# Kernel tuning notes

Hardware: AMD Instinct MI355X
Metric: run time of the kernel (lower is better)

Reference implementation:

```python
import jax, jax.numpy as jnp
import numpy as np
import math

E = 8192        # number of hyperedges in the batch
IN_DIM = 256
OUT_DIM = 128


def setup_inputs() -> dict:
    key = jax.random.key(0)
    k1, k2, k3, k4 = jax.random.split(key, 4)
    node_embeddings = jax.random.normal(k1, (E, IN_DIM), dtype=jnp.float32)
    # xavier_uniform-like scale for the projection weights
    lim = 1.414 * math.sqrt(6.0 / (IN_DIM + OUT_DIM))
    query_weight = jax.random.uniform(k2, (IN_DIM, OUT_DIM), minval=-lim, maxval=lim, dtype=jnp.float32)
    key_weight = jax.random.uniform(k3, (IN_DIM, OUT_DIM), minval=-lim, maxval=lim, dtype=jnp.float32)
    # binary hypergraph connectivity mask [E, E]; diagonal forced to 1 so no row is fully masked
    mask = jax.random.randint(k4, (E, E), 0, 2, dtype=jnp.int32)
    mask = mask.at[jnp.arange(E), jnp.arange(E)].set(1)
    return {
        "node_embeddings": node_embeddings,
        "query_weight": query_weight,
        "key_weight": key_weight,
        "attention_mask": mask,
    }


def reference(node_embeddings, query_weight, key_weight, attention_mask):
    # QK projections: [E, in] x [in, out] -> [E, out]
    q = node_embeddings @ query_weight
    k = node_embeddings @ key_weight
    # scaled scores [E, E]
    scores = (q @ k.T) / jnp.sqrt(jnp.asarray(OUT_DIM, dtype=q.dtype))
    # masked_fill(mask == 0, -inf)
    scores = jnp.where(attention_mask == 0, jnp.asarray(-jnp.inf, dtype=scores.dtype), scores)
    probs = jax.nn.softmax(scores, axis=1)
    # output aggregates the KEY projections (as in the original code)
    return probs @ k
```

## Files before the change

### kernel.cpp

```cpp
#include <hip/hip_runtime.h>
#include <stdint.h>

#define E_N 8192
#define SPLIT 8
#define CH 16
#define QBLK 64

typedef unsigned short u16;
typedef unsigned int u32;
typedef unsigned long long u64;
typedef __attribute__((ext_vector_type(4))) float f32x4;
typedef __attribute__((ext_vector_type(8))) short bf16x8;
typedef __attribute__((ext_vector_type(4))) unsigned int u32x4;
typedef __attribute__((ext_vector_type(2))) unsigned int u32x2;

union V16 { u32x4 q; bf16x8 h; u16 u[8]; };

static __device__ __forceinline__ u16 f2bf(float f) {
  union { float f; unsigned u; } c; c.f = f;
  unsigned r = c.u + 0x7FFFu + ((c.u >> 16) & 1u);
  return (u16)(r >> 16);
}

constexpr float QS = 1.4426950408889634f / 11.313708498984761f;

__global__ void k_wt(const float* __restrict__ Wq, const float* __restrict__ Wk,
                     u16* __restrict__ wt) {
  int idx = blockIdx.x * 256 + threadIdx.x;
  int mat = idx >> 15, rem = idx & 32767;
  float v = mat ? Wk[rem] : Wq[rem];
  int d = rem >> 7, c = rem & 127;
  wt[(mat * 128 + c) * 256 + d] = f2bf(v);
}

__launch_bounds__(256)
__global__ void k_proj(const float* __restrict__ X, const u16* __restrict__ wt,
                       u16* __restrict__ qg, u16* __restrict__ kg) {
  __shared__ __align__(16) char Xs[64 * 512];
  const int tid = threadIdx.x;
  const int wid = tid >> 6, lane = tid & 63, g = lane >> 4, l15 = lane & 15;
  const int r0 = blockIdx.x * 64;
#pragma unroll
  for (int i = 0; i < 16; ++i) {
    int s = tid + 256 * i;
    int row = s >> 6, c4 = (s & 63) << 2;
    f32x4 v = *(const f32x4*)(X + (size_t)(r0 + row) * 256 + c4);
    u32x2 pk;
    pk[0] = f2bf(v[0]) | ((unsigned)f2bf(v[1]) << 16);
    pk[1] = f2bf(v[2]) | ((unsigned)f2bf(v[3]) << 16);
    *(u32x2*)(Xs + (((row << 9) + (c4 << 1)) ^ ((row & 7) << 4))) = pk;
  }
  __syncthreads();
  bf16x8 xa[8];
  const int arow = wid * 16 + l15;
#pragma unroll
  for (int ks = 0; ks < 8; ++ks) {
    V16 t; t.q = *(const u32x4*)(Xs + (((arow << 9) + (ks << 6) + (g << 4)) ^ ((l15 & 7) << 4)));
    xa[ks] = t.h;
  }
  const f32x4 zero4 = {0.f, 0.f, 0.f, 0.f};
  f32x4 acc[16];
#pragma unroll
  for (int i = 0; i < 16; ++i) acc[i] = zero4;
#pragma unroll
  for (int ct = 0; ct < 16; ++ct) {
    int mat = ct >> 3, c = ((ct & 7) << 4) + l15;
#pragma unroll
    for (int ks = 0; ks < 8; ++ks) {
      V16 b; b.q = *(const u32x4*)(wt + ((mat * 128 + c) * 256 + (ks << 5) + (g << 3)));
      acc[ct] = __builtin_amdgcn_mfma_f32_16x16x32_bf16(xa[ks], b.h, acc[ct], 0, 0, 0);
    }
  }
#pragma unroll
  for (int ct = 0; ct < 16; ++ct) {
    int mat = ct >> 3, c = ((ct & 7) << 4) + l15;
#pragma unroll
    for (int r = 0; r < 4; ++r) {
      int row = r0 + wid * 16 + 4 * g + r;
      float v = acc[ct][r];
      if (mat == 0) qg[row * 128 + c] = f2bf(v * QS);
      else          kg[row * 128 + c] = f2bf(v);
    }
  }
}

__global__ void k_kt(const u16* __restrict__ kg, u16* __restrict__ ktg) {
  __shared__ __align__(16) u16 Ts[64 * 66];
  const int tid = threadIdx.x;
  const int b = blockIdx.x;
  const int r0 = (b >> 1) * 64, c0 = (b & 1) * 64;
#pragma unroll
  for (int i = 0; i < 2; ++i) {
    int s = tid + 256 * i;
    int row = s >> 3, seg = s & 7;
    u32x4 v = *(const u32x4*)(kg + (size_t)(r0 + row) * 128 + c0 + seg * 8);
    unsigned* dst = (unsigned*)((char*)Ts + row * 132 + seg * 16);
    dst[0] = v[0]; dst[1] = v[1]; dst[2] = v[2]; dst[3] = v[3];
  }
  __syncthreads();
#pragma unroll
  for (int i = 0; i < 2; ++i) {
    int s = tid + 256 * i;
    int oc = s >> 3, seg2 = s & 7;
    u16 t[8];
#pragma unroll
    for (int j = 0; j < 8; ++j) t[j] = Ts[(seg2 * 8 + j) * 66 + oc];
    u32x4 o;
    o[0] = t[0] | ((unsigned)t[1] << 16);
    o[1] = t[2] | ((unsigned)t[3] << 16);
    o[2] = t[4] | ((unsigned)t[5] << 16);
    o[3] = t[6] | ((unsigned)t[7] << 16);
    *(u32x4*)(ktg + (size_t)(c0 + oc) * E_N + r0 + seg2 * 8) = o;
  }
}

#define BARRIER() { asm volatile("s_waitcnt lgkmcnt(0)" ::: "memory"); \
                    __builtin_amdgcn_s_barrier(); }

#define LOADREGS(KV1)                                                           \
  {                                                                             \
    const u16* kp = kgp + (size_t)(KV1) * 128;                                  \
    kr0 = *(const u32x4*)(kp);                                                  \
    kr1 = *(const u32x4*)(kp + 16 * 128);                                       \
    kr2 = *(const u32x4*)(kp + 32 * 128);                                       \
    kr3 = *(const u32x4*)(kp + 48 * 128);                                       \
    const u16* tp = ktp + (KV1);                                                \
    tr0 = *(const u32x4*)(tp);                                                  \
    tr1 = *(const u32x4*)(tp + 32 * E_N);                                       \
    tr2 = *(const u32x4*)(tp + 64 * E_N);                                       \
    tr3 = *(const u32x4*)(tp + 96 * E_N);                                       \
  }

#define WRITELDS(KW, TW)                                                        \
  {                                                                             \
    *(u32x4*)((KW) + kofs)          = kr0;                                      \
    *(u32x4*)((KW) + kofs + 4096)   = kr1;                                      \
    *(u32x4*)((KW) + kofs + 8192)   = kr2;                                      \
    *(u32x4*)((KW) + kofs + 12288)  = kr3;                                      \
    *(u32x4*)((TW) + tofs)          = tr0;                                      \
    *(u32x4*)((TW) + tofs + 4096)   = tr1;                                      \
    *(u32x4*)((TW) + tofs + 8192)   = tr2;                                      \
    *(u32x4*)((TW) + tofs + 12288)  = tr3;                                      \
  }

#define MASKLOAD(SET, KV1)                                                      \
  {                                                                             \
    _Pragma("unroll")                                                           \
    for (int s4 = 0; s4 < 4; ++s4)                                              \
      SET[s4] = *(const u32x4*)(mbase + (size_t)(s4 * 4) * E_N + (KV1));        \
  }

#define MASKBALLOT(SET, PH)                                                     \
  {                                                                             \
    u32 mlo = 0, mhi = 0;                                                       \
    _Pragma("unroll")                                                           \
    for (int s4 = 0; s4 < 4; ++s4) {                                            \
      _Pragma("unroll")                                                         \
      for (int c = 0; c < 4; ++c) {                                             \
        u64 b = __ballot(SET[s4][c] != 0);                                      \
        if (lane == s4 * 4 + c) { mlo = (u32)b; mhi = (u32)(b >> 32); }         \
      }                                                                         \
    }                                                                           \
    if (lane < 16) { u32x2 o; o[0] = mlo; o[1] = mhi;                           \
      *(u32x2*)(MshW + (PH) * 32 + lane * 2) = o; }                             \
  }

#define FSTEP(SUB, KR, TR, KW, TW, LSET, BSET, DOP, DOB, DOW)                   \
  {                                                                             \
    if (DOP) {                                                                  \
      const int kvm = kvbase + (((st2 + (SUB) + 2 + qb) & 15) << 6);            \
      MASKLOAD(LSET, kvm)                                                       \
    }                                                                           \
    u32 wlo, whi;                                                               \
    { u32x2 t3 = *(const u32x2*)(MshW + (SUB) * 32 + (g * 4 + (l15 & 3)) * 2);  \
      wlo = t3[0]; whi = t3[1]; }                                               \
    f32x4 S[4];                                                                 \
    _Pragma("unroll")                                                           \
    for (int t = 0; t < 4; ++t) S[t] = zero4;                                   \
    _Pragma("unroll")                                                           \
    for (int t = 0; t < 4; ++t) {                                               \
      int krow = t * 16 + l15;                                                  \
      _Pragma("unroll")                                                         \
      for (int ks = 0; ks < 4; ++ks) {                                          \
        V16 kf; kf.q = *(const u32x4*)((KR) + (((krow << 8) + (ks << 6) + (g << 4)) ^ ((l15 & 7) << 4))); \
        S[t] = __builtin_amdgcn_mfma_f32_16x16x32_bf16(qf[ks], kf.h, S[t], 0, 0, 0); \
      }                                                                         \
    }                                                                           \
    _Pragma("unroll")                                                           \
    for (int t = 0; t < 4; ++t) {                                               \
      _Pragma("unroll")                                                         \
      for (int r = 0; r < 4; ++r) {                                             \
        u32 w = (r & 2) ? whi : wlo;                                            \
        float pv = ((w >> ((r & 1) * 16 + t * 4 + q2)) & 1u)                    \
                       ? __builtin_amdgcn_exp2f(S[t][r]) : 0.f;                 \
        lacc[r] += pv;                                                          \
        int prow = 4 * g + r;                                                   \
        *(u16*)(Pw + ((prow * 128 + (t * 16 + l15) * 2) ^ ((prow & 7) << 4))) = f2bf(pv); \
      }                                                                         \
    }                                                                           \
    bf16x8 pa0, pa1;                                                            \
    { V16 t2; t2.q = *(const u32x4*)(Pw + ((l15 * 128 + g * 16) ^ ((l15 & 7) << 4))); pa0 = t2.h; } \
    { V16 t2; t2.q = *(const u32x4*)(Pw + ((l15 * 128 + 64 + g * 16) ^ ((l15 & 7) << 4))); pa1 = t2.h; } \
    _Pragma("unroll")                                                           \
    for (int dt = 0; dt < 8; ++dt) {                                            \
      int krow = dt * 16 + l15;                                                 \
      V16 kf0; kf0.q = *(const u32x4*)((TR) + (((krow << 7) + (g << 4)) ^ ((l15 & 7) << 4))); \
      Oacc[dt] = __builtin_amdgcn_mfma_f32_16x16x32_bf16(pa0, kf0.h, Oacc[dt], 0, 0, 0); \
      V16 kf1; kf1.q = *(const u32x4*)((TR) + (((krow << 7) + 64 + (g << 4)) ^ ((l15 & 7) << 4))); \
      Oacc[dt] = __builtin_amdgcn_mfma_f32_16x16x32_bf16(pa1, kf1.h, Oacc[dt], 0, 0, 0); \
    }                                                                           \
    if (DOB) MASKBALLOT(BSET, 1 - (SUB))                                        \
    if (DOW) WRITELDS(KW, TW)                                                   \
    if (DOP) {                                                                  \
      const int kvt = kvbase + (((st2 + (SUB) + 2 + qb) & 15) << 6);            \
      LOADREGS(kvt)                                                             \
    }                                                                           \
    if (DOW) BARRIER()                                                          \
  }

__launch_bounds__(256, 2)
__global__ void k_flash(const u16* __restrict__ qg, const u16* __restrict__ kg,
                        const u16* __restrict__ ktg, const int* __restrict__ M,
                        float* __restrict__ Op, float* __restrict__ lp) {
  __shared__ __align__(16) char K0[64 * 256], K1[64 * 256];
  __shared__ __align__(16) char T0[128 * 128], T1[128 * 128];
  __shared__ __align__(16) char Psh[4 * 2048];
  __shared__ __align__(8)  u32 Msh[4][2][32];
  const int tid = threadIdx.x;
  const int wid = tid >> 6, lane = tid & 63, g = lane >> 4, l15 = lane & 15;
  const int q2 = l15 >> 2;
  const int bid = blockIdx.x;
  const int split = bid & 7, qb = bid >> 3;
  const int qb0 = qb * QBLK;
  const int kvbase = split * (E_N / SPLIT);
  char* Pw = Psh + wid * 2048;
  u32* const MshW = &Msh[wid][0][0];
  const int* mbase = M + (size_t)(qb0 + wid * 16 + (lane >> 4)) * E_N + 4 * (lane & 15);
  u32x4 mqa[4], mqb[4];

  const int kr_r = tid >> 4, kr_s = tid & 15;
  const int tr_d = tid >> 3, tr_s = tid & 7;
  const int kofs = ((kr_r << 8) + (kr_s << 4)) ^ ((kr_r & 7) << 4);
  const int tofs = ((tr_d << 7) + (tr_s << 4)) ^ ((tr_d & 7) << 4);
  const u16* kgp = kg + (size_t)kr_r * 128 + kr_s * 8;
  const u16* ktp = ktg + (size_t)tr_d * E_N + tr_s * 8;
  u32x4 kr0, kr1, kr2, kr3, tr0, tr1, tr2, tr3;

  bf16x8 qf[4];
  {
    const u16* qrow = qg + (size_t)(qb0 + wid * 16 + l15) * 128;
#pragma unroll
    for (int ks = 0; ks < 4; ++ks) {
      V16 t; t.q = *(const u32x4*)(qrow + (ks << 5) + (g << 3));
      qf[ks] = t.h;
    }
  }
  const f32x4 zero4 = {0.f, 0.f, 0.f, 0.f};
  f32x4 Oacc[8];
#pragma unroll
  for (int i = 0; i < 8; ++i) Oacc[i] = zero4;
  float lacc[4] = {0.f, 0.f, 0.f, 0.f};

  {
    const int c0 = kvbase + ((qb & 15) << 6);
    const int c1 = kvbase + (((qb + 1) & 15) << 6);
    MASKLOAD(mqa, c0)
    MASKLOAD(mqb, c1)
    LOADREGS(c0)
    MASKBALLOT(mqa, 0)
    WRITELDS(K0, T0)
    LOADREGS(c1)
    BARRIER()
  }

  for (int st2 = 0; st2 < CH; st2 += 2) {
    FSTEP(0, K0, T0, K1, T1, mqa, mqb, (st2 < 14), true, true)
    FSTEP(1, K1, T1, K0, T0, mqb, mqa, (st2 < 14), (st2 < 14), (st2 < 14))
  }

#pragma unroll
  for (int r = 0; r < 4; ++r) {
    float v = lacc[r];
    v += __shfl_xor(v, 1);
    v += __shfl_xor(v, 2);
    v += __shfl_xor(v, 4);
    v += __shfl_xor(v, 8);
    lacc[r] = v;
  }
  if (l15 == 0) {
#pragma unroll
    for (int r = 0; r < 4; ++r)
      lp[split * E_N + qb0 + wid * 16 + 4 * g + r] = lacc[r];
  }
  float* op = Op + ((size_t)split * E_N + qb0 + wid * 16) * 128;
#pragma unroll
  for (int dt = 0; dt < 8; ++dt)
#pragma unroll
    for (int r = 0; r < 4; ++r)
      op[(4 * g + r) * 128 + dt * 16 + l15] = Oacc[dt][r];
}

__global__ void k_comb(const float* __restrict__ Op, const float* __restrict__ lp,
                       float* __restrict__ out) {
  int idx4 = blockIdx.x * 256 + threadIdx.x;
  int base = idx4 << 2;
  int e = base >> 7;
  f32x4 o = {0.f, 0.f, 0.f, 0.f};
  float l = 0.f;
#pragma unroll
  for (int s = 0; s < SPLIT; ++s) {
    o += *(const f32x4*)(Op + (size_t)s * (E_N * 128) + base);
    l += lp[s * E_N + e];
  }
  float rl = 1.0f / l;
  o[0] *= rl; o[1] *= rl; o[2] *= rl; o[3] *= rl;
  *(f32x4*)(out + base) = o;
}

extern "C" void kernel_launch(void* const* d_in, const int* in_sizes, int n_in,
                              void* d_out, int out_size, void* d_ws, size_t ws_size,
                              hipStream_t stream) {
  const float* X  = (const float*)d_in[0];
  const float* Wq = (const float*)d_in[1];
  const float* Wk = (const float*)d_in[2];
  const int*   M  = (const int*)d_in[3];
  char* ws = (char*)d_ws;
  u16*   qg   = (u16*)(ws);
  u16*   kg   = (u16*)(ws + (size_t)(2u << 20));
  u16*   ktg  = (u16*)(ws + (size_t)(4u << 20));
  u16*   wt   = (u16*)(ws + (size_t)(6u << 20));
  float* lp   = (float*)(ws + (size_t)(6u << 20) + (128u << 10));
  float* Op   = (float*)(ws + (size_t)(6u << 20) + (512u << 10) + (8u << 20));
  float* out = (float*)d_out;

  k_wt  <<<256, 256, 0, stream>>>(Wq, Wk, wt);
  k_proj<<<128, 256, 0, stream>>>(X, wt, qg, kg);
  k_kt  <<<256, 256, 0, stream>>>(kg, ktg);
  k_flash<<<SPLIT * (E_N / QBLK), 256, 0, stream>>>(qg, kg, ktg, M, Op, lp);
  k_comb<<<(E_N * 128 / 4) / 256, 256, 0, stream>>>(Op, lp, out);
}
```

Baseline: 123.3 us.

## Transpose score MFMA so each lane reads its mask directly, drop ballot staging

Swaps the MFMA operand order so each lane holds scores for one query row and four consecutive key columns. That lets each lane load its own int32 mask values straight from global memory and test them per element. This removes the ballot-based bitmask packing through shared memory and the per-element bit extraction. P values are now written to LDS as packed 4-element stores, and the row-sum reduction collapses to a single accumulator with two shuffles. The trade-off is that mask loads now hold 16 u32x4 registers per set, so register pressure may rise, and the mask loads are rescheduled to fetch both sets at once.

```diff
diff --git a/kernel.cpp b/kernel.cpp
--- a/kernel.cpp
+++ b/kernel.cpp
@@ -146,34 +146,12 @@
 #define MASKLOAD(SET, KV1)                                                      \
   {                                                                             \
     _Pragma("unroll")                                                           \
-    for (int s4 = 0; s4 < 4; ++s4)                                              \
-      SET[s4] = *(const u32x4*)(mbase + (size_t)(s4 * 4) * E_N + (KV1));        \
-  }
-
-#define MASKBALLOT(SET, PH)                                                     \
+    for (int t4 = 0; t4 < 4; ++t4)                                              \
+      SET[t4] = *(const u32x4*)(mrow + (KV1) + t4 * 16);                        \
+  }
+
+#define FSTEP(SUB, KR, TR, KW, TW, MSET, DOM, DOP, DOW)                         \
   {                                                                             \
-    u32 mlo = 0, mhi = 0;                                                       \
-    _Pragma("unroll")                                                           \
-    for (int s4 = 0; s4 < 4; ++s4) {                                            \
-      _Pragma("unroll")                                                         \
-      for (int c = 0; c < 4; ++c) {                                             \
-        u64 b = __ballot(SET[s4][c] != 0);                                      \
-        if (lane == s4 * 4 + c) { mlo = (u32)b; mhi = (u32)(b >> 32); }         \
-      }                                                                         \
-    }                                                                           \
-    if (lane < 16) { u32x2 o; o[0] = mlo; o[1] = mhi;                           \
-      *(u32x2*)(MshW + (PH) * 32 + lane * 2) = o; }                             \
-  }
-
-#define FSTEP(SUB, KR, TR, KW, TW, LSET, BSET, DOP, DOB, DOW)                   \
-  {                                                                             \
-    if (DOP) {                                                                  \
-      const int kvm = kvbase + (((st2 + (SUB) + 2 + qb) & 15) << 6);            \
-      MASKLOAD(LSET, kvm)                                                       \
-    }                                                                           \
-    u32 wlo, whi;                                                               \
-    { u32x2 t3 = *(const u32x2*)(MshW + (SUB) * 32 + (g * 4 + (l15 & 3)) * 2);  \
-      wlo = t3[0]; whi = t3[1]; }                                               \
     f32x4 S[4];                                                                 \
     _Pragma("unroll")                                                           \
     for (int t = 0; t < 4; ++t) S[t] = zero4;                                   \
@@ -183,20 +161,24 @@
       _Pragma("unroll")                                                         \
       for (int ks = 0; ks < 4; ++ks) {                                          \
         V16 kf; kf.q = *(const u32x4*)((KR) + (((krow << 8) + (ks << 6) + (g << 4)) ^ ((l15 & 7) << 4))); \
-        S[t] = __builtin_amdgcn_mfma_f32_16x16x32_bf16(qf[ks], kf.h, S[t], 0, 0, 0); \
+        S[t] = __builtin_amdgcn_mfma_f32_16x16x32_bf16(kf.h, qf[ks], S[t], 0, 0, 0); \
       }                                                                         \
     }                                                                           \
     _Pragma("unroll")                                                           \
     for (int t = 0; t < 4; ++t) {                                               \
-      _Pragma("unroll")                                                         \
-      for (int r = 0; r < 4; ++r) {                                             \
-        u32 w = (r & 2) ? whi : wlo;                                            \
-        float pv = ((w >> ((r & 1) * 16 + t * 4 + q2)) & 1u)                    \
-                       ? __builtin_amdgcn_exp2f(S[t][r]) : 0.f;                 \
-        lacc[r] += pv;                                                          \
-        int prow = 4 * g + r;                                                   \
-        *(u16*)(Pw + ((prow * 128 + (t * 16 + l15) * 2) ^ ((prow & 7) << 4))) = f2bf(pv); \
-      }                                                                         \
+      float p0 = MSET[t][0] ? __builtin_amdgcn_exp2f(S[t][0]) : 0.f;            \
+      float p1 = MSET[t][1] ? __builtin_amdgcn_exp2f(S[t][1]) : 0.f;            \
+      float p2 = MSET[t][2] ? __builtin_amdgcn_exp2f(S[t][2]) : 0.f;            \
+      float p3 = MSET[t][3] ? __builtin_amdgcn_exp2f(S[t][3]) : 0.f;            \
+      lacc += (p0 + p1) + (p2 + p3);                                            \
+      u32x2 pk;                                                                 \
+      pk[0] = f2bf(p0) | ((u32)f2bf(p1) << 16);                                 \
+      pk[1] = f2bf(p2) | ((u32)f2bf(p3) << 16);                                 \
+      *(u32x2*)(Pw + ((l15 * 128 + (t * 16 + 4 * g) * 2) ^ ((l15 & 7) << 4))) = pk; \
+    }                                                                           \
+    if (DOM) {                                                                  \
+      MASKLOAD(mqa, kvbase + (((st2 + 2 + qb) & 15) << 6))                      \
+      MASKLOAD(mqb, kvbase + (((st2 + 3 + qb) & 15) << 6))                      \
     }                                                                           \
     bf16x8 pa0, pa1;                                                            \
     { V16 t2; t2.q = *(const u32x4*)(Pw + ((l15 * 128 + g * 16) ^ ((l15 & 7) << 4))); pa0 = t2.h; } \
@@ -209,7 +191,6 @@
       V16 kf1; kf1.q = *(const u32x4*)((TR) + (((krow << 7) + 64 + (g << 4)) ^ ((l15 & 7) << 4))); \
       Oacc[dt] = __builtin_amdgcn_mfma_f32_16x16x32_bf16(pa1, kf1.h, Oacc[dt], 0, 0, 0); \
     }                                                                           \
-    if (DOB) MASKBALLOT(BSET, 1 - (SUB))                                        \
     if (DOW) WRITELDS(KW, TW)                                                   \
     if (DOP) {                                                                  \
       const int kvt = kvbase + (((st2 + (SUB) + 2 + qb) & 15) << 6);            \
@@ -225,17 +206,14 @@
   __shared__ __align__(16) char K0[64 * 256], K1[64 * 256];
   __shared__ __align__(16) char T0[128 * 128], T1[128 * 128];
   __shared__ __align__(16) char Psh[4 * 2048];
-  __shared__ __align__(8)  u32 Msh[4][2][32];
   const int tid = threadIdx.x;
   const int wid = tid >> 6, lane = tid & 63, g = lane >> 4, l15 = lane & 15;
-  const int q2 = l15 >> 2;
   const int bid = blockIdx.x;
   const int split = bid & 7, qb = bid >> 3;
   const int qb0 = qb * QBLK;
   const int kvbase = split * (E_N / SPLIT);
   char* Pw = Psh + wid * 2048;
-  u32* const MshW = &Msh[wid][0][0];
-  const int* mbase = M + (size_t)(qb0 + wid * 16 + (lane >> 4)) * E_N + 4 * (lane & 15);
+  const u32* mrow = (const u32*)M + (size_t)(qb0 + wid * 16 + l15) * E_N + 4 * g;
   u32x4 mqa[4], mqb[4];
 
   const int kr_r = tid >> 4, kr_s = tid & 15;
@@ -259,38 +237,30 @@
   f32x4 Oacc[8];
 #pragma unroll
   for (int i = 0; i < 8; ++i) Oacc[i] = zero4;
-  float lacc[4] = {0.f, 0.f, 0.f, 0.f};
+  float lacc = 0.f;
 
   {
-    const int c0 = kvbase + ((qb & 15) << 6);
-    const int c1 = kvbase + (((qb + 1) & 15) << 6);
-    MASKLOAD(mqa, c0)
-    MASKLOAD(mqb, c1)
-    LOADREGS(c0)
-    MASKBALLOT(mqa, 0)
+    const int c0 = (qb & 15) << 6;
+    const int c1 = ((qb + 1) & 15) << 6;
+    MASKLOAD(mqa, kvbase + c0)
+    MASKLOAD(mqb, kvbase + c1)
+    LOADREGS(kvbase + c0)
     WRITELDS(K0, T0)
-    LOADREGS(c1)
+    LOADREGS(kvbase + c1)
     BARRIER()
   }
 
   for (int st2 = 0; st2 < CH; st2 += 2) {
-    FSTEP(0, K0, T0, K1, T1, mqa, mqb, (st2 < 14), true, true)
-    FSTEP(1, K1, T1, K0, T0, mqb, mqa, (st2 < 14), (st2 < 14), (st2 < 14))
-  }
-
-#pragma unroll
-  for (int r = 0; r < 4; ++r) {
-    float v = lacc[r];
-    v += __shfl_xor(v, 1);
-    v += __shfl_xor(v, 2);
-    v += __shfl_xor(v, 4);
-    v += __shfl_xor(v, 8);
-    lacc[r] = v;
-  }
-  if (l15 == 0) {
-#pragma unroll
-    for (int r = 0; r < 4; ++r)
-      lp[split * E_N + qb0 + wid * 16 + 4 * g + r] = lacc[r];
+    FSTEP(0, K0, T0, K1, T1, mqa, false, (st2 < 14), true)
+    FSTEP(1, K1, T1, K0, T0, mqb, (st2 < 14), (st2 < 14), (st2 < 14))
+  }
+
+  {
+    float v = lacc;
+    v += __shfl_xor(v, 16);
+    v += __shfl_xor(v, 32);
+    if (lane < 16)
+      lp[split * E_N + qb0 + wid * 16 + lane] = v;
   }
   float* op = Op + ((size_t)split * E_N + qb0 + wid * 16) * 128;
 #pragma unroll
```

Result: no change. 122.4 us (-0.7%).
